# Kernel optimization log

Hardware: AMD Instinct MI355X
Metric: run time of the kernel (lower is better)

Reference implementation:

```python
import jax, jax.numpy as jnp
import numpy as np
import math

D_MODEL = 1024
N_HEADS = 16
D_HEAD = D_MODEL // N_HEADS
MAX_SEQ_LEN = 2048
BASE = 10000.0


def _rope_tables(L):
    pos = jnp.arange(L, dtype=jnp.float32)[:, None]                      # [L,1]
    freqs = jnp.exp(-math.log(BASE) * jnp.arange(0, D_HEAD, 2, dtype=jnp.float32) / D_HEAD)  # [d/2]
    angles = pos * freqs                                                  # [L, d/2]
    return jnp.sin(angles), jnp.cos(angles)


def _apply_rope(x, sin, cos):
    # x: [B, L, H, d_head], interleaved even/odd rotation
    s = sin[None, :, None, :]
    c = cos[None, :, None, :]
    x_even, x_odd = x[..., ::2], x[..., 1::2]
    rot_even = x_even * c - x_odd * s
    rot_odd = x_even * s + x_odd * c
    # re-interleave: stack on new last axis then flatten
    return jnp.stack([rot_even, rot_odd], axis=-1).reshape(x.shape)


def setup_inputs() -> dict:
    key = jax.random.key(0)
    k0, k1, k2, k3, k4 = jax.random.split(key, 5)
    B, L = 2, 2048
    scale = 1.0 / math.sqrt(D_MODEL)
    return {
        "x": jax.random.normal(k0, (B, L, D_MODEL), dtype=jnp.float32),
        "W_q": jax.random.normal(k1, (D_MODEL, D_MODEL), dtype=jnp.float32) * scale,
        "W_k": jax.random.normal(k2, (D_MODEL, D_MODEL), dtype=jnp.float32) * scale,
        "W_v": jax.random.normal(k3, (D_MODEL, D_MODEL), dtype=jnp.float32) * scale,
        "W_o": jax.random.normal(k4, (D_MODEL, D_MODEL), dtype=jnp.float32) * scale,
    }


def reference(x, W_q, W_k, W_v, W_o):
    B, L, _ = x.shape
    sin, cos = _rope_tables(L)
    # nn.Linear(no bias): y = x @ W.T
    q = (x @ W_q.T).reshape(B, L, N_HEADS, D_HEAD)
    k = (x @ W_k.T).reshape(B, L, N_HEADS, D_HEAD)
    v = (x @ W_v.T).reshape(B, L, N_HEADS, D_HEAD)
    q = _apply_rope(q, sin, cos)
    k = _apply_rope(k, sin, cos)
    scores = jnp.einsum('blhd,bshd->bhls', q, k) / math.sqrt(D_HEAD)
    weights = jax.nn.softmax(scores, axis=-1)
    out = jnp.einsum('bhls,bshd->blhd', weights, v).reshape(B, L, D_MODEL)
    return out @ W_o.T
```

## Files before the change

kernel.cpp:

```cpp
#include <hip/hip_runtime.h>
#include <hip/hip_bf16.h>
#include <math.h>

typedef __bf16 bf16_t;
typedef __bf16 bf16x8 __attribute__((ext_vector_type(8)));
typedef __bf16 bf16x4 __attribute__((ext_vector_type(4)));
typedef float  f32x4  __attribute__((ext_vector_type(4)));
typedef float  f32x16 __attribute__((ext_vector_type(16)));
typedef unsigned u32x4 __attribute__((ext_vector_type(4)));

#define D_MODEL 1024
#define NH      16
#define DH      64
#define LSEQ    2048
#define NROWS   4096
#define LOG2E   1.44269504088896340736f
#define SHIFT_L2 17.312340490667562f

__device__ __forceinline__ void gld_lds16(bf16_t* lds, const bf16_t* g) {
  __builtin_amdgcn_global_load_lds(
      (__attribute__((address_space(1))) void*)(unsigned long long)g,
      (__attribute__((address_space(3))) void*)lds,
      16, 0, 0);
}

__device__ __forceinline__ unsigned cvtpk_bf16(float lo, float hi) {
  unsigned r;
  asm("v_cvt_pk_bf16_f32 %0, %1, %2" : "=v"(r) : "v"(lo), "v"(hi));
  return r;
}

__device__ __forceinline__ void pl32swap(unsigned& a, unsigned& b) {
  asm volatile("v_permlane32_swap_b32 %0, %1" : "+v"(a), "+v"(b));
}

__global__ __launch_bounds__(256)
void k_cvt(const float* __restrict__ in, bf16_t* __restrict__ out, int n4) {
  int i = blockIdx.x * blockDim.x + threadIdx.x;
  int stride = gridDim.x * blockDim.x;
  for (; i < n4; i += stride) {
    float4 v = ((const float4*)in)[i];
    bf16x4 o = { (bf16_t)v.x, (bf16_t)v.y, (bf16_t)v.z, (bf16_t)v.w };
    ((bf16x4*)out)[i] = o;
  }
}

__global__ __launch_bounds__(256)
void k_cvtw(const float* __restrict__ w0, const float* __restrict__ w1,
            const float* __restrict__ w2, const float* __restrict__ w3,
            bf16_t* __restrict__ out) {
  int i = blockIdx.x * blockDim.x + threadIdx.x;
  int src = i >> 18;
  const float* w = (src == 0) ? w0 : (src == 1) ? w1 : (src == 2) ? w2 : w3;
  float4 v = ((const float4*)w)[i & 262143];
  bf16x4 o = { (bf16_t)v.x, (bf16_t)v.y, (bf16_t)v.z, (bf16_t)v.w };
  ((bf16x4*)out)[i] = o;
}

__global__ __launch_bounds__(256)
void k_tab(float2* __restrict__ tab) {
  int i = blockIdx.x * blockDim.x + threadIdx.x;
  int l = i >> 5, p = i & 31;
  float freq = expf(-0.28782313662425575f * (float)p);
  float s, c;
  sincosf((float)l * freq, &s, &c);
  tab[i] = make_float2(c, s);
}

__global__ __launch_bounds__(256)
void k_gemm_qkv(const bf16_t* __restrict__ A, const bf16_t* __restrict__ B,
                bf16_t* __restrict__ Qo, bf16_t* __restrict__ Ko, bf16_t* __restrict__ Vo,
                const float2* __restrict__ tab)
{
  __shared__ bf16_t As[3][128 * 32];
  __shared__ bf16_t Bs[3][128 * 32];
  const int tid  = threadIdx.x;
  const int wave = tid >> 6, lane = tid & 63;
  const int hi   = lane >> 4, lo = lane & 15;
  const int m0   = blockIdx.y * 128, n0 = blockIdx.x * 128;
  const int wr   = (wave >> 1) * 64, wc = (wave & 1) * 64;

  const bf16_t* Ap0 = A + (size_t)(m0 + (tid >> 2)) * 1024 + (tid & 3) * 8;
  const bf16_t* Ap1 = Ap0 + (size_t)64 * 1024;
  const bf16_t* Bp0 = B + (size_t)(n0 + (tid >> 2)) * 1024 + (tid & 3) * 8;
  const bf16_t* Bp1 = Bp0 + (size_t)64 * 1024;

  auto stage = [&](int buf) {
    gld_lds16(&As[buf][tid * 8], Ap0);
    gld_lds16(&As[buf][2048 + tid * 8], Ap1);
    gld_lds16(&Bs[buf][tid * 8], Bp0);
    gld_lds16(&Bs[buf][2048 + tid * 8], Bp1);
    Ap0 += 32; Ap1 += 32; Bp0 += 32; Bp1 += 32;
  };

  f32x4 acc[4][4] = {};

  auto compute = [&](int buf) {
    bf16x8 a[4], b[4];
    #pragma unroll
    for (int mi = 0; mi < 4; mi++)
      a[mi] = *(const bf16x8*)(&As[buf][(wr + mi * 16 + lo) * 32 + hi * 8]);
    #pragma unroll
    for (int ni = 0; ni < 4; ni++)
      b[ni] = *(const bf16x8*)(&Bs[buf][(wc + ni * 16 + lo) * 32 + hi * 8]);
    __builtin_amdgcn_s_setprio(1);
    #pragma unroll
    for (int mi = 0; mi < 4; mi++)
      #pragma unroll
      for (int ni = 0; ni < 4; ni++)
        acc[mi][ni] = __builtin_amdgcn_mfma_f32_16x16x32_bf16(a[mi], b[ni], acc[mi][ni], 0, 0, 0);
    __builtin_amdgcn_s_setprio(0);
  };

  stage(0);
  stage(1);
  #pragma unroll 1
  for (int t = 0; t < 30; ++t) {
    asm volatile("s_waitcnt vmcnt(4)" ::: "memory");
    __builtin_amdgcn_sched_barrier(0);
    __builtin_amdgcn_s_barrier();
    __builtin_amdgcn_sched_barrier(0);
    stage((t + 2) % 3);
    compute(t % 3);
  }
  asm volatile("s_waitcnt vmcnt(4)" ::: "memory");
  __builtin_amdgcn_sched_barrier(0);
  __builtin_amdgcn_s_barrier();
  __builtin_amdgcn_sched_barrier(0);
  compute(0);
  asm volatile("s_waitcnt vmcnt(0)" ::: "memory");
  __builtin_amdgcn_sched_barrier(0);
  __builtin_amdgcn_s_barrier();
  __builtin_amdgcn_sched_barrier(0);
  compute(1);

  #pragma unroll
  for (int mi = 0; mi < 4; mi++)
    #pragma unroll
    for (int ni = 0; ni < 4; ni++)
      #pragma unroll
      for (int r = 0; r < 4; r++) {
        float val  = acc[mi][ni][r];
        float part = __shfl_xor(val, 1, 64);
        int row = m0 + wr + mi * 16 + hi * 4 + r;
        int col = n0 + wc + ni * 16 + lo;
        int which = col >> 10;
        int h = (col >> 6) & 15;
        int d = col & 63;
        int b = row >> 11, l = row & 2047;
        size_t oidx = ((size_t)(b * NH + h) * LSEQ + l) * DH + d;
        if (which == 2) {
          Vo[oidx] = (bf16_t)val;
        } else {
          float2 sc = tab[l * 32 + (d >> 1)];
          float rot = (d & 1) ? (part * sc.y + val * sc.x) : (val * sc.x - part * sc.y);
          if (which == 0) rot *= 0.125f * LOG2E;
          (which == 0 ? Qo : Ko)[oidx] = (bf16_t)rot;
        }
      }
}

__global__ __launch_bounds__(256)
void k_gemm_o(const bf16_t* __restrict__ A, const bf16_t* __restrict__ B,
              int N, int K, float* __restrict__ Fo)
{
  __shared__ bf16_t As[128 * 32];
  __shared__ bf16_t Bs[128 * 32];
  const int tid  = threadIdx.x;
  const int wave = tid >> 6, lane = tid & 63;
  const int hi   = lane >> 4, lo = lane & 15;
  const int m0   = blockIdx.y * 128, n0 = blockIdx.x * 128;
  const int wr   = (wave >> 1) * 64, wc = (wave & 1) * 64;

  f32x4 acc[4][4] = {};

  for (int k0 = 0; k0 < K; k0 += 32) {
    __syncthreads();
    {
      int id = tid;
      gld_lds16(As + id * 8, A + (size_t)(m0 + (id >> 2)) * K + k0 + (id & 3) * 8);
      gld_lds16(Bs + id * 8, B + (size_t)(n0 + (id >> 2)) * K + k0 + (id & 3) * 8);
      id = tid + 256;
      gld_lds16(As + id * 8, A + (size_t)(m0 + (id >> 2)) * K + k0 + (id & 3) * 8);
      gld_lds16(Bs + id * 8, B + (size_t)(n0 + (id >> 2)) * K + k0 + (id & 3) * 8);
    }
    __syncthreads();

    bf16x8 a[4], b[4];
    #pragma unroll
    for (int mi = 0; mi < 4; mi++)
      a[mi] = *(const bf16x8*)(As + (wr + mi * 16 + lo) * 32 + hi * 8);
    #pragma unroll
    for (int ni = 0; ni < 4; ni++)
      b[ni] = *(const bf16x8*)(Bs + (wc + ni * 16 + lo) * 32 + hi * 8);
    #pragma unroll
    for (int mi = 0; mi < 4; mi++)
      #pragma unroll
      for (int ni = 0; ni < 4; ni++)
        acc[mi][ni] = __builtin_amdgcn_mfma_f32_16x16x32_bf16(a[mi], b[ni], acc[mi][ni], 0, 0, 0);
  }

  #pragma unroll
  for (int mi = 0; mi < 4; mi++)
    #pragma unroll
    for (int ni = 0; ni < 4; ni++)
      #pragma unroll
      for (int r = 0; r < 4; r++) {
        int row = m0 + wr + mi * 16 + hi * 4 + r;
        int col = n0 + wc + ni * 16 + lo;
        Fo[(size_t)row * N + col] = acc[mi][ni][r];
      }
}

__global__ __launch_bounds__(256)
void k_vt(const bf16_t* __restrict__ Vrm, bf16_t* __restrict__ VT) {
  __shared__ bf16_t T[64][66];
  const int tid = threadIdx.x;
  const int bh = blockIdx.y, l0 = blockIdx.x * 64;
  const bf16_t* src = Vrm + ((size_t)bh * LSEQ + l0) * DH;
  #pragma unroll
  for (int pass = 0; pass < 2; pass++) {
    int chunk = tid + pass * 256;
    int row = chunk >> 3, slot = chunk & 7;
    bf16x8 v = *(const bf16x8*)(src + row * DH + slot * 8);
    #pragma unroll
    for (int j = 0; j < 8; j++) T[slot * 8 + j][row] = v[j];
  }
  __syncthreads();
  bf16_t* dst = VT + (size_t)bh * DH * LSEQ + l0;
  #pragma unroll
  for (int pass = 0; pass < 2; pass++) {
    int chunk = tid + pass * 256;
    int d = chunk >> 3, slot = chunk & 7;
    bf16x8 v;
    #pragma unroll
    for (int j = 0; j < 8; j++) v[j] = T[d][slot * 8 + j];
    *(bf16x8*)(dst + (size_t)d * LSEQ + slot * 8) = v;
  }
}

__global__ __launch_bounds__(1024)
void k_attn(const bf16_t* __restrict__ Q, const bf16_t* __restrict__ K,
            const bf16_t* __restrict__ VT, bf16_t* __restrict__ O)
{
  __shared__ __align__(16) bf16_t smem[49152];
  const int tid  = threadIdx.x;
  const int wave = tid >> 6, lane = tid & 63;
  const int kg   = wave & 1;
  const int qg   = wave >> 1;
  const int ql   = lane & 31;
  const int hi   = lane >> 5;
  const int bh = blockIdx.x;
  const int qblock = blockIdx.y * 256 + qg * 32;

  bf16_t* kbase = smem + kg * 3 * 4096;
  bf16_t* vbase = smem + 24576 + kg * 3 * 4096;

  const bf16_t* Qb = Q + (size_t)bh * LSEQ * DH;

  bf16x8 qf[4];
  #pragma unroll
  for (int s = 0; s < 4; s++)
    qf[s] = *(const bf16x8*)(Qb + (size_t)(qblock + ql) * DH + s * 16 + hi * 8);

  const int r0 = qg * 8 + (lane >> 3), s0l = lane & 7;
  const int swo = (s0l ^ (r0 & 7)) * 8;
  const bf16_t* kgp = K  + ((size_t)bh * LSEQ + kg * 1024 + r0) * DH + swo;
  const bf16_t* vgp = VT + ((size_t)bh * DH + r0) * LSEQ + kg * 1024 + swo;
  const int dstoff = qg * 512 + lane * 8;

  auto stage = [&](int buf) {
    gld_lds16(kbase + buf * 4096 + dstoff, kgp);
    gld_lds16(vbase + buf * 4096 + dstoff, vgp);
    kgp += 64 * DH; vgp += 64;
  };

  f32x16 acc[2] = {};
  float lrun = 0.f;

  f32x16 shinit;
  #pragma unroll
  for (int r = 0; r < 16; r++) shinit[r] = -SHIFT_L2;

  auto compute = [&](const bf16_t* Kbuf, const bf16_t* Vbuf) {
    const char* Kcur = (const char*)Kbuf;
    f32x16 st[2] = { shinit, shinit };
    __builtin_amdgcn_s_setprio(1);
    #pragma unroll
    for (int kt = 0; kt < 2; kt++) {
      int row = kt * 32 + ql;
      int swz = (row & 7) << 4;
      #pragma unroll
      for (int s = 0; s < 4; s++) {
        bf16x8 ka = *(const bf16x8*)(Kcur + row * 128 + ((s * 32 + hi * 16) ^ swz));
        st[kt] = __builtin_amdgcn_mfma_f32_32x32x16_bf16(ka, qf[s], st[kt], 0, 0, 0);
      }
    }
    __builtin_amdgcn_s_setprio(0);

    float p[32];
    float rs = 0.f;
    #pragma unroll
    for (int kt = 0; kt < 2; kt++)
      #pragma unroll
      for (int r = 0; r < 16; r++) {
        float e = __builtin_amdgcn_exp2f(st[kt][r]);
        p[kt * 16 + r] = e;
        rs += e;
      }
    lrun += rs;

    bf16x8 pa[4];
    #pragma unroll
    for (int g = 0; g < 4; g++) {
      unsigned a0 = cvtpk_bf16(p[g * 8 + 0], p[g * 8 + 1]);
      unsigned b0 = cvtpk_bf16(p[g * 8 + 4], p[g * 8 + 5]);
      pl32swap(a0, b0);
      unsigned a1 = cvtpk_bf16(p[g * 8 + 2], p[g * 8 + 3]);
      unsigned b1 = cvtpk_bf16(p[g * 8 + 6], p[g * 8 + 7]);
      pl32swap(a1, b1);
      union { u32x4 u; bf16x8 h; } w;
      w.u[0] = a0; w.u[1] = a1; w.u[2] = b0; w.u[3] = b1;
      pa[g] = w.h;
    }

    const char* Vcur = (const char*)Vbuf;
    __builtin_amdgcn_s_setprio(1);
    #pragma unroll
    for (int dt = 0; dt < 2; dt++) {
      int row = dt * 32 + ql;
      int swz = (row & 7) << 4;
      #pragma unroll
      for (int ks = 0; ks < 4; ks++) {
        bf16x8 va = *(const bf16x8*)(Vcur + row * 128 + ((ks * 32 + hi * 16) ^ swz));
        acc[dt] = __builtin_amdgcn_mfma_f32_32x32x16_bf16(va, pa[ks], acc[dt], 0, 0, 0);
      }
    }
    __builtin_amdgcn_s_setprio(0);
  };

  stage(0);
  stage(1);
  #pragma unroll 1
  for (int t = 0; t < 14; ++t) {
    asm volatile("s_waitcnt vmcnt(2)" ::: "memory");
    __builtin_amdgcn_sched_barrier(0);
    __builtin_amdgcn_s_barrier();
    __builtin_amdgcn_sched_barrier(0);
    stage((t + 2) % 3);
    compute(kbase + (t % 3) * 4096, vbase + (t % 3) * 4096);
  }
  asm volatile("s_waitcnt vmcnt(2)" ::: "memory");
  __builtin_amdgcn_sched_barrier(0);
  __builtin_amdgcn_s_barrier();
  __builtin_amdgcn_sched_barrier(0);
  compute(kbase + 2 * 4096, vbase + 2 * 4096);
  asm volatile("s_waitcnt vmcnt(0)" ::: "memory");
  __builtin_amdgcn_sched_barrier(0);
  __builtin_amdgcn_s_barrier();
  __builtin_amdgcn_sched_barrier(0);
  compute(kbase, vbase);

  __syncthreads();
  float* xch = (float*)smem;
  float* px = xch + (qg * 64 + lane) * 34;
  if (kg == 1) {
    #pragma unroll
    for (int r = 0; r < 16; r++) { px[r] = acc[0][r]; px[16 + r] = acc[1][r]; }
    px[32] = lrun;
  }
  __syncthreads();
  if (kg == 0) {
    #pragma unroll
    for (int r = 0; r < 16; r++) { acc[0][r] += px[r]; acc[1][r] += px[16 + r]; }
    lrun += px[32];
    float lfull = lrun + __shfl_xor(lrun, 32, 64);
    float inv = 1.0f / lfull;
    const int b = bh >> 4, h = bh & 15;
    const int lpos = qblock + ql;
    #pragma unroll
    for (int dt = 0; dt < 2; dt++)
      #pragma unroll
      for (int r = 0; r < 16; r++) {
        int d = dt * 32 + (r & 3) + 8 * (r >> 2) + 4 * hi;
        O[(size_t)(b * LSEQ + lpos) * D_MODEL + h * DH + d] = (bf16_t)(acc[dt][r] * inv);
      }
  }
}

extern "C" void kernel_launch(void* const* d_in, const int* in_sizes, int n_in,
                              void* d_out, int out_size, void* d_ws, size_t ws_size,
                              hipStream_t stream)
{
  (void)in_sizes; (void)n_in; (void)out_size; (void)ws_size;
  const float* x  = (const float*)d_in[0];
  const float* Wq = (const float*)d_in[1];
  const float* Wk = (const float*)d_in[2];
  const float* Wv = (const float*)d_in[3];
  const float* Wo = (const float*)d_in[4];
  float* out = (float*)d_out;

  bf16_t* ws   = (bf16_t*)d_ws;
  bf16_t* xb   = ws;
  bf16_t* wqkv = xb + (size_t)NROWS * D_MODEL;
  bf16_t* wo   = wqkv + (size_t)3 * D_MODEL * D_MODEL;
  bf16_t* Qw   = wo + (size_t)D_MODEL * D_MODEL;
  bf16_t* Kw   = Qw + (size_t)NROWS * D_MODEL;
  bf16_t* Vw   = Kw + (size_t)NROWS * D_MODEL;
  bf16_t* VTw  = Vw + (size_t)NROWS * D_MODEL;
  bf16_t* Aw   = VTw + (size_t)NROWS * D_MODEL;
  float2* tab  = (float2*)(Aw + (size_t)NROWS * D_MODEL);

  k_tab<<<256, 256, 0, stream>>>(tab);
  k_cvt<<<1024, 256, 0, stream>>>(x, xb, NROWS * D_MODEL / 4);
  k_cvtw<<<4096, 256, 0, stream>>>(Wq, Wk, Wv, Wo, wqkv);

  dim3 g1(3072 / 128, 4096 / 128);
  k_gemm_qkv<<<g1, 256, 0, stream>>>(xb, wqkv, Qw, Kw, Vw, tab);

  dim3 gv(LSEQ / 64, 32);
  k_vt<<<gv, 256, 0, stream>>>(Vw, VTw);

  dim3 g2(32, LSEQ / 256);
  k_attn<<<g2, 1024, 0, stream>>>(Qw, Kw, VTw, Aw);

  dim3 g3(1024 / 128, 4096 / 128);
  k_gemm_o<<<g3, 256, 0, stream>>>(Aw, wo, 1024, 1024, out);
}
```

Baseline: 133.6 us.

## Merge prep kernels and unify GEMMs into 512-thread triple-buffered template

Fuses the three preprocessing kernels (x conversion, weight conversion, RoPE table) into one launch to cut launch overhead. Replaces the QKV and output-projection GEMMs with a single templated kernel using 512 threads (8 waves, each computing a 32x64 sub-tile) and a triple-buffered global_load_lds pipeline. The output projection thereby gains the pipelined loading it lacked. Smaller per-wave tiles reduce register use and raise occupancy, at the cost of less MFMA reuse per LDS fragment load.

Result: faster. 118.9 us (-11.0%).

```diff
diff --git a/kernel.cpp b/kernel.cpp
--- a/kernel.cpp
+++ b/kernel.cpp
@@ -35,42 +35,40 @@
 }
 
 __global__ __launch_bounds__(256)
-void k_cvt(const float* __restrict__ in, bf16_t* __restrict__ out, int n4) {
-  int i = blockIdx.x * blockDim.x + threadIdx.x;
-  int stride = gridDim.x * blockDim.x;
-  for (; i < n4; i += stride) {
-    float4 v = ((const float4*)in)[i];
+void k_prep(const float* __restrict__ x,
+            const float* __restrict__ w0, const float* __restrict__ w1,
+            const float* __restrict__ w2, const float* __restrict__ w3,
+            bf16_t* __restrict__ xb, bf16_t* __restrict__ wout, float2* __restrict__ tab)
+{
+  int gid = blockIdx.x * 256 + threadIdx.x;
+  if (gid < 1048576) {
+    float4 v = ((const float4*)x)[gid];
     bf16x4 o = { (bf16_t)v.x, (bf16_t)v.y, (bf16_t)v.z, (bf16_t)v.w };
-    ((bf16x4*)out)[i] = o;
-  }
-}
-
-__global__ __launch_bounds__(256)
-void k_cvtw(const float* __restrict__ w0, const float* __restrict__ w1,
-            const float* __restrict__ w2, const float* __restrict__ w3,
-            bf16_t* __restrict__ out) {
-  int i = blockIdx.x * blockDim.x + threadIdx.x;
-  int src = i >> 18;
-  const float* w = (src == 0) ? w0 : (src == 1) ? w1 : (src == 2) ? w2 : w3;
-  float4 v = ((const float4*)w)[i & 262143];
-  bf16x4 o = { (bf16_t)v.x, (bf16_t)v.y, (bf16_t)v.z, (bf16_t)v.w };
-  ((bf16x4*)out)[i] = o;
-}
-
-__global__ __launch_bounds__(256)
-void k_tab(float2* __restrict__ tab) {
-  int i = blockIdx.x * blockDim.x + threadIdx.x;
-  int l = i >> 5, p = i & 31;
-  float freq = expf(-0.28782313662425575f * (float)p);
-  float s, c;
-  sincosf((float)l * freq, &s, &c);
-  tab[i] = make_float2(c, s);
-}
-
-__global__ __launch_bounds__(256)
-void k_gemm_qkv(const bf16_t* __restrict__ A, const bf16_t* __restrict__ B,
-                bf16_t* __restrict__ Qo, bf16_t* __restrict__ Ko, bf16_t* __restrict__ Vo,
-                const float2* __restrict__ tab)
+    ((bf16x4*)xb)[gid] = o;
+  } else if (gid < 2097152) {
+    int i = gid - 1048576;
+    int src = i >> 18;
+    const float* w = (src == 0) ? w0 : (src == 1) ? w1 : (src == 2) ? w2 : w3;
+    float4 v = ((const float4*)w)[i & 262143];
+    bf16x4 o = { (bf16_t)v.x, (bf16_t)v.y, (bf16_t)v.z, (bf16_t)v.w };
+    ((bf16x4*)wout)[i] = o;
+  } else if (gid < 2162688) {
+    int i = gid - 2097152;
+    int l = i >> 5, p = i & 31;
+    float freq = expf(-0.28782313662425575f * (float)p);
+    float s, c;
+    sincosf((float)l * freq, &s, &c);
+    tab[i] = make_float2(c, s);
+  }
+}
+
+template<int MODE>
+__global__ __launch_bounds__(512, 6)
+void k_gemm(const bf16_t* __restrict__ A, const bf16_t* __restrict__ B,
+            int N, int K,
+            float* __restrict__ Fo,
+            bf16_t* __restrict__ Qo, bf16_t* __restrict__ Ko, bf16_t* __restrict__ Vo,
+            const float2* __restrict__ tab)
 {
   __shared__ bf16_t As[3][128 * 32];
   __shared__ bf16_t Bs[3][128 * 32];
@@ -78,138 +76,96 @@
   const int wave = tid >> 6, lane = tid & 63;
   const int hi   = lane >> 4, lo = lane & 15;
   const int m0   = blockIdx.y * 128, n0 = blockIdx.x * 128;
-  const int wr   = (wave >> 1) * 64, wc = (wave & 1) * 64;
-
-  const bf16_t* Ap0 = A + (size_t)(m0 + (tid >> 2)) * 1024 + (tid & 3) * 8;
-  const bf16_t* Ap1 = Ap0 + (size_t)64 * 1024;
-  const bf16_t* Bp0 = B + (size_t)(n0 + (tid >> 2)) * 1024 + (tid & 3) * 8;
-  const bf16_t* Bp1 = Bp0 + (size_t)64 * 1024;
+  const int wr2  = (wave >> 1) * 32, wc2 = (wave & 1) * 64;
+
+  const bf16_t* Ap = A + (size_t)(m0 + (tid >> 2)) * K + (tid & 3) * 8;
+  const bf16_t* Bp = B + (size_t)(n0 + (tid >> 2)) * K + (tid & 3) * 8;
 
   auto stage = [&](int buf) {
-    gld_lds16(&As[buf][tid * 8], Ap0);
-    gld_lds16(&As[buf][2048 + tid * 8], Ap1);
-    gld_lds16(&Bs[buf][tid * 8], Bp0);
-    gld_lds16(&Bs[buf][2048 + tid * 8], Bp1);
-    Ap0 += 32; Ap1 += 32; Bp0 += 32; Bp1 += 32;
+    gld_lds16(&As[buf][tid * 8], Ap);
+    gld_lds16(&Bs[buf][tid * 8], Bp);
+    Ap += 32; Bp += 32;
   };
 
-  f32x4 acc[4][4] = {};
+  f32x4 acc[2][4] = {};
 
   auto compute = [&](int buf) {
-    bf16x8 a[4], b[4];
-    #pragma unroll
-    for (int mi = 0; mi < 4; mi++)
-      a[mi] = *(const bf16x8*)(&As[buf][(wr + mi * 16 + lo) * 32 + hi * 8]);
+    bf16x8 a[2], b[4];
+    #pragma unroll
+    for (int mi = 0; mi < 2; mi++)
+      a[mi] = *(const bf16x8*)(&As[buf][(wr2 + mi * 16 + lo) * 32 + hi * 8]);
     #pragma unroll
     for (int ni = 0; ni < 4; ni++)
-      b[ni] = *(const bf16x8*)(&Bs[buf][(wc + ni * 16 + lo) * 32 + hi * 8]);
+      b[ni] = *(const bf16x8*)(&Bs[buf][(wc2 + ni * 16 + lo) * 32 + hi * 8]);
     __builtin_amdgcn_s_setprio(1);
     #pragma unroll
-    for (int mi = 0; mi < 4; mi++)
+    for (int mi = 0; mi < 2; mi++)
       #pragma unroll
       for (int ni = 0; ni < 4; ni++)
         acc[mi][ni] = __builtin_amdgcn_mfma_f32_16x16x32_bf16(a[mi], b[ni], acc[mi][ni], 0, 0, 0);
     __builtin_amdgcn_s_setprio(0);
   };
 
+  const int nt = K >> 5;
   stage(0);
   stage(1);
   #pragma unroll 1
-  for (int t = 0; t < 30; ++t) {
-    asm volatile("s_waitcnt vmcnt(4)" ::: "memory");
+  for (int t = 0; t < nt - 2; ++t) {
+    asm volatile("s_waitcnt vmcnt(2)" ::: "memory");
     __builtin_amdgcn_sched_barrier(0);
     __builtin_amdgcn_s_barrier();
     __builtin_amdgcn_sched_barrier(0);
     stage((t + 2) % 3);
     compute(t % 3);
   }
-  asm volatile("s_waitcnt vmcnt(4)" ::: "memory");
+  asm volatile("s_waitcnt vmcnt(2)" ::: "memory");
   __builtin_amdgcn_sched_barrier(0);
   __builtin_amdgcn_s_barrier();
   __builtin_amdgcn_sched_barrier(0);
-  compute(0);
+  compute((nt - 2) % 3);
   asm volatile("s_waitcnt vmcnt(0)" ::: "memory");
   __builtin_amdgcn_sched_barrier(0);
   __builtin_amdgcn_s_barrier();
   __builtin_amdgcn_sched_barrier(0);
-  compute(1);
-
-  #pragma unroll
-  for (int mi = 0; mi < 4; mi++)
-    #pragma unroll
-    for (int ni = 0; ni < 4; ni++)
-      #pragma unroll
-      for (int r = 0; r < 4; r++) {
-        float val  = acc[mi][ni][r];
-        float part = __shfl_xor(val, 1, 64);
-        int row = m0 + wr + mi * 16 + hi * 4 + r;
-        int col = n0 + wc + ni * 16 + lo;
-        int which = col >> 10;
-        int h = (col >> 6) & 15;
-        int d = col & 63;
-        int b = row >> 11, l = row & 2047;
-        size_t oidx = ((size_t)(b * NH + h) * LSEQ + l) * DH + d;
-        if (which == 2) {
-          Vo[oidx] = (bf16_t)val;
-        } else {
-          float2 sc = tab[l * 32 + (d >> 1)];
-          float rot = (d & 1) ? (part * sc.y + val * sc.x) : (val * sc.x - part * sc.y);
-          if (which == 0) rot *= 0.125f * LOG2E;
-          (which == 0 ? Qo : Ko)[oidx] = (bf16_t)rot;
+  compute((nt - 1) % 3);
+
+  if constexpr (MODE == 0) {
+    #pragma unroll
+    for (int mi = 0; mi < 2; mi++)
+      #pragma unroll
+      for (int ni = 0; ni < 4; ni++)
+        #pragma unroll
+        for (int r = 0; r < 4; r++) {
+          int row = m0 + wr2 + mi * 16 + hi * 4 + r;
+          int col = n0 + wc2 + ni * 16 + lo;
+          Fo[(size_t)row * N + col] = acc[mi][ni][r];
         }
-      }
-}
-
-__global__ __launch_bounds__(256)
-void k_gemm_o(const bf16_t* __restrict__ A, const bf16_t* __restrict__ B,
-              int N, int K, float* __restrict__ Fo)
-{
-  __shared__ bf16_t As[128 * 32];
-  __shared__ bf16_t Bs[128 * 32];
-  const int tid  = threadIdx.x;
-  const int wave = tid >> 6, lane = tid & 63;
-  const int hi   = lane >> 4, lo = lane & 15;
-  const int m0   = blockIdx.y * 128, n0 = blockIdx.x * 128;
-  const int wr   = (wave >> 1) * 64, wc = (wave & 1) * 64;
-
-  f32x4 acc[4][4] = {};
-
-  for (int k0 = 0; k0 < K; k0 += 32) {
-    __syncthreads();
-    {
-      int id = tid;
-      gld_lds16(As + id * 8, A + (size_t)(m0 + (id >> 2)) * K + k0 + (id & 3) * 8);
-      gld_lds16(Bs + id * 8, B + (size_t)(n0 + (id >> 2)) * K + k0 + (id & 3) * 8);
-      id = tid + 256;
-      gld_lds16(As + id * 8, A + (size_t)(m0 + (id >> 2)) * K + k0 + (id & 3) * 8);
-      gld_lds16(Bs + id * 8, B + (size_t)(n0 + (id >> 2)) * K + k0 + (id & 3) * 8);
-    }
-    __syncthreads();
-
-    bf16x8 a[4], b[4];
-    #pragma unroll
-    for (int mi = 0; mi < 4; mi++)
-      a[mi] = *(const bf16x8*)(As + (wr + mi * 16 + lo) * 32 + hi * 8);
-    #pragma unroll
-    for (int ni = 0; ni < 4; ni++)
-      b[ni] = *(const bf16x8*)(Bs + (wc + ni * 16 + lo) * 32 + hi * 8);
-    #pragma unroll
-    for (int mi = 0; mi < 4; mi++)
+  } else {
+    #pragma unroll
+    for (int mi = 0; mi < 2; mi++)
       #pragma unroll
       for (int ni = 0; ni < 4; ni++)
-        acc[mi][ni] = __builtin_amdgcn_mfma_f32_16x16x32_bf16(a[mi], b[ni], acc[mi][ni], 0, 0, 0);
-  }
-
-  #pragma unroll
-  for (int mi = 0; mi < 4; mi++)
-    #pragma unroll
-    for (int ni = 0; ni < 4; ni++)
-      #pragma unroll
-      for (int r = 0; r < 4; r++) {
-        int row = m0 + wr + mi * 16 + hi * 4 + r;
-        int col = n0 + wc + ni * 16 + lo;
-        Fo[(size_t)row * N + col] = acc[mi][ni][r];
-      }
+        #pragma unroll
+        for (int r = 0; r < 4; r++) {
+          float val  = acc[mi][ni][r];
+          float part = __shfl_xor(val, 1, 64);
+          int row = m0 + wr2 + mi * 16 + hi * 4 + r;
+          int col = n0 + wc2 + ni * 16 + lo;
+          int which = col >> 10;
+          int h = (col >> 6) & 15;
+          int d = col & 63;
+          int b = row >> 11, l = row & 2047;
+          size_t oidx = ((size_t)(b * NH + h) * LSEQ + l) * DH + d;
+          if (which == 2) {
+            Vo[oidx] = (bf16_t)val;
+          } else {
+            float2 sc = tab[l * 32 + (d >> 1)];
+            float rot = (d & 1) ? (part * sc.y + val * sc.x) : (val * sc.x - part * sc.y);
+            if (which == 0) rot *= 0.125f * LOG2E;
+            (which == 0 ? Qo : Ko)[oidx] = (bf16_t)rot;
+          }
+        }
+  }
 }
 
 __global__ __launch_bounds__(256)
@@ -411,12 +367,10 @@
   bf16_t* Aw   = VTw + (size_t)NROWS * D_MODEL;
   float2* tab  = (float2*)(Aw + (size_t)NROWS * D_MODEL);
 
-  k_tab<<<256, 256, 0, stream>>>(tab);
-  k_cvt<<<1024, 256, 0, stream>>>(x, xb, NROWS * D_MODEL / 4);
-  k_cvtw<<<4096, 256, 0, stream>>>(Wq, Wk, Wv, Wo, wqkv);
+  k_prep<<<8448, 256, 0, stream>>>(x, Wq, Wk, Wv, Wo, xb, wqkv, tab);
 
   dim3 g1(3072 / 128, 4096 / 128);
-  k_gemm_qkv<<<g1, 256, 0, stream>>>(xb, wqkv, Qw, Kw, Vw, tab);
+  k_gemm<1><<<g1, 512, 0, stream>>>(xb, wqkv, 3072, 1024, nullptr, Qw, Kw, Vw, tab);
 
   dim3 gv(LSEQ / 64, 32);
   k_vt<<<gv, 256, 0, stream>>>(Vw, VTw);
@@ -425,5 +379,5 @@
   k_attn<<<g2, 1024, 0, stream>>>(Qw, Kw, VTw, Aw);
 
   dim3 g3(1024 / 128, 4096 / 128);
-  k_gemm_o<<<g3, 256, 0, stream>>>(Aw, wo, 1024, 1024, out);
-}
+  k_gemm<0><<<g3, 512, 0, stream>>>(Aw, wo, 1024, 1024, out, nullptr, nullptr, nullptr, nullptr);
+}
```
